# Kernel tuning notes

Measured on AMD Instinct MI355X. Metric: run time of the kernel, lower is better.

The kernel has to match this reference:

```python
import jax, jax.numpy as jnp
import numpy as np


def setup_inputs() -> dict:
    key = jax.random.key(0)
    kq, kk, kv = jax.random.split(key, 3)
    B, H, S, D = 4, 16, 2048, 64
    Q = jax.random.normal(kq, (B, H, S, D), dtype=jnp.float32)
    K = jax.random.normal(kk, (B, H, S, D), dtype=jnp.float32)
    V = jax.random.normal(kv, (B, H, S, D), dtype=jnp.float32)
    return {"Q": Q, "K": K, "V": V}


def reference(Q, K, V):
    # Faithful to the source: scale = d**(-2); scores = (Q @ K^T) / scale
    # i.e. scores are MULTIPLIED by d^2 (quirk of the original module).
    d = K.shape[-1]
    scale = jnp.asarray(d, Q.dtype) ** (-2)
    scores = jnp.einsum('bhqd,bhkd->bhqk', Q, K) / scale  # [B,H,S,S]
    attn = jax.nn.softmax(scores, axis=-1)
    out = jnp.einsum('bhqk,bhkd->bhqd', attn, V)
    return out
```

## Files before the change

### kernel.cpp

```cpp
#include <hip/hip_runtime.h>
#include <math.h>


#define S_LEN 2048
#define D_DIM 64
#define NH 64
#define BM 128
#define BN 64
#define QTILES (S_LEN / BM)
#define KTILES (S_LEN / BN)

typedef unsigned short u16;
typedef unsigned int u32;
typedef _Float16 f16;
typedef __attribute__((ext_vector_type(8))) _Float16 f16x8;
typedef __attribute__((ext_vector_type(2))) __fp16 fp16x2;
typedef __attribute__((ext_vector_type(4))) float f32x4;

#define SC_FULL (4096.0f * 1.4426950408889634f)
#define QSCALE (SC_FULL / 64.0f)
#define KSCALE 64.0f

union f16cv { f16 h; u16 u; };
union pkcv { fp16x2 h; u32 u; };

__device__ __forceinline__ void split2h(float a, u16& hi, u16& lo) {
  f16cv ch, cl;
  ch.h = (f16)a;
  float r = a - (float)ch.h;
  cl.h = (f16)r;
  hi = ch.u; lo = cl.u;
}

__device__ __forceinline__ int swz(int row, int chunk) {
  return (row << 6) + ((chunk ^ (row & 7)) << 3);
}

__global__ void prep_kernel(const float* __restrict__ K, const float* __restrict__ V,
                            u16* __restrict__ Kh, u16* __restrict__ Km,
                            u16* __restrict__ Vt) {
  if (blockIdx.x < 8192) {
    size_t i4 = ((size_t)blockIdx.x * 256 + threadIdx.x) * 4;
    float4 v = *(const float4*)(K + i4);
    u16 h0, l0, h1, l1, h2, l2, h3, l3;
    split2h(v.x * KSCALE, h0, l0);
    split2h(v.y * KSCALE, h1, l1);
    split2h(v.z * KSCALE, h2, l2);
    split2h(v.w * KSCALE, h3, l3);
    *(uint2*)(Kh + i4) = make_uint2((u32)h0 | ((u32)h1 << 16), (u32)h2 | ((u32)h3 << 16));
    *(uint2*)(Km + i4) = make_uint2((u32)l0 | ((u32)l1 << 16), (u32)l2 | ((u32)l3 << 16));
  } else {
    __shared__ float Vf[64 * 65];
    const int idx = blockIdx.x - 8192;
    const int kt = idx & 31, h = idx >> 5;
    const int tid = threadIdx.x;
    const float* V0 = V + ((size_t)h * S_LEN + kt * 64) * 64;
    const int tx = tid & 15, ty = tid >> 4;
#pragma unroll
    for (int p = 0; p < 4; ++p) {
      int r = ty + 16 * p;
      float4 v = *(const float4*)(V0 + r * 64 + tx * 4);
      Vf[r * 65 + 4 * tx + 0] = v.x;
      Vf[r * 65 + 4 * tx + 1] = v.y;
      Vf[r * 65 + 4 * tx + 2] = v.z;
      Vf[r * 65 + 4 * tx + 3] = v.w;
    }
    __syncthreads();
    const int ch = tid & 7, dr = tid >> 3;
#pragma unroll
    for (int p = 0; p < 2; ++p) {
      int d = dr + 32 * p;
      u32 w[4];
#pragma unroll
      for (int i = 0; i < 4; ++i) {
        f16cv a, b;
        a.h = (f16)Vf[(8 * ch + 2 * i) * 65 + d];
        b.h = (f16)Vf[(8 * ch + 2 * i + 1) * 65 + d];
        w[i] = (u32)a.u | ((u32)b.u << 16);
      }
      size_t o = ((size_t)h * 64 + d) * S_LEN + (size_t)kt * 64 + 8 * ch;
      *(uint4*)(Vt + o) = make_uint4(w[0], w[1], w[2], w[3]);
    }
  }
}

#define K0_B 0
#define K1_B 4096
#define VT_B 8192
#define P_B  12288
#define LDS_USH 20480

__global__ __launch_bounds__(256, 3)
void attn_mfma_f16(const float* __restrict__ Q, const u16* __restrict__ Kh,
                   const u16* __restrict__ Km, const u16* __restrict__ Vt,
                   float* __restrict__ O) {
  __shared__ __align__(16) u16 lds[LDS_USH];

  const int tid = threadIdx.x;
  const int lane = tid & 63;
  const int wv = tid >> 6;
  const int c = lane & 15;
  const int g = lane >> 4;
  const int h = blockIdx.x;
  const int qtile = blockIdx.y;

  f16x8 aqh[2][2], aqm[2][2];
#pragma unroll
  for (int m = 0; m < 2; ++m) {
    int qrow = qtile * BM + wv * 32 + m * 16 + c;
    const float* qp = Q + ((size_t)h * S_LEN + qrow) * 64 + g * 8;
#pragma unroll
    for (int ks = 0; ks < 2; ++ks) {
      float4 a = *(const float4*)(qp + ks * 32);
      float4 b = *(const float4*)(qp + ks * 32 + 4);
      float v[8] = {a.x, a.y, a.z, a.w, b.x, b.y, b.z, b.w};
      f16x8 hi, lo;
#pragma unroll
      for (int e = 0; e < 8; ++e) {
        float q = v[e] * QSCALE;
        f16 qh = (f16)q;
        hi[e] = qh;
        lo[e] = (f16)(q - (float)qh);
      }
      aqh[m][ks] = hi; aqm[m][ks] = lo;
    }
  }

  f32x4 Oacc[2][4];
  float mrow[2] = {-INFINITY, -INFINITY};
  float lrow[2] = {0.f, 0.f};
#pragma unroll
  for (int m = 0; m < 2; ++m)
#pragma unroll
    for (int t = 0; t < 4; ++t) Oacc[m][t] = (f32x4){0.f, 0.f, 0.f, 0.f};

  const int srow = tid >> 2;
  const int c0 = tid & 3;
  const int d0a = swz(srow, c0), d0b = swz(srow, c0 + 4);
  const size_t gKbase = ((size_t)h * S_LEN + srow) * 64 + c0 * 8;
  const size_t gVbase = ((size_t)h * 64 + srow) * S_LEN + c0 * 8;

  uint4 rk0a = *(const uint4*)(Kh + gKbase);
  uint4 rk0b = *(const uint4*)(Kh + gKbase + 32);
  uint4 rk1a = *(const uint4*)(Km + gKbase);
  uint4 rk1b = *(const uint4*)(Km + gKbase + 32);
  uint4 rva  = *(const uint4*)(Vt + gVbase);
  uint4 rvb  = *(const uint4*)(Vt + gVbase + 32);

  for (int kt = 0; kt < KTILES; ++kt) {
    __syncthreads();
    *(uint4*)&lds[K0_B + d0a] = rk0a;
    *(uint4*)&lds[K0_B + d0b] = rk0b;
    *(uint4*)&lds[K1_B + d0a] = rk1a;
    *(uint4*)&lds[K1_B + d0b] = rk1b;
    *(uint4*)&lds[VT_B + d0a] = rva;
    *(uint4*)&lds[VT_B + d0b] = rvb;
    __syncthreads();

    if (kt + 1 < KTILES) {
      size_t gK = gKbase + (size_t)(kt + 1) * BN * 64;
      size_t gV = gVbase + (size_t)(kt + 1) * BN;
      rk0a = *(const uint4*)(Kh + gK);
      rk0b = *(const uint4*)(Kh + gK + 32);
      rk1a = *(const uint4*)(Km + gK);
      rk1b = *(const uint4*)(Km + gK + 32);
      rva  = *(const uint4*)(Vt + gV);
      rvb  = *(const uint4*)(Vt + gV + 32);
    }

    f32x4 S[2][4];
#pragma unroll
    for (int m = 0; m < 2; ++m)
#pragma unroll
      for (int t = 0; t < 4; ++t) S[m][t] = (f32x4){0.f, 0.f, 0.f, 0.f};
#pragma unroll
    for (int ks = 0; ks < 2; ++ks) {
#pragma unroll
      for (int t = 0; t < 4; ++t) {
        int off = swz(16 * t + c, g + 4 * ks);
        f16x8 bh = *(const f16x8*)&lds[K0_B + off];
        f16x8 bm = *(const f16x8*)&lds[K1_B + off];
#pragma unroll
        for (int m = 0; m < 2; ++m) {
          S[m][t] = __builtin_amdgcn_mfma_f32_16x16x32_f16(bh, aqh[m][ks], S[m][t], 0, 0, 0);
          S[m][t] = __builtin_amdgcn_mfma_f32_16x16x32_f16(bm, aqh[m][ks], S[m][t], 0, 0, 0);
          S[m][t] = __builtin_amdgcn_mfma_f32_16x16x32_f16(bh, aqm[m][ks], S[m][t], 0, 0, 0);
        }
      }
    }

#pragma unroll
    for (int m = 0; m < 2; ++m) {
      float mx = S[m][0][0];
#pragma unroll
      for (int t = 0; t < 4; ++t)
#pragma unroll
        for (int r = 0; r < 4; ++r) mx = fmaxf(mx, S[m][t][r]);
      mx = fmaxf(mx, __shfl_xor(mx, 16));
      mx = fmaxf(mx, __shfl_xor(mx, 32));
      float mnew = fmaxf(mrow[m], mx);
      float a = exp2f(mrow[m] - mnew);
      mrow[m] = mnew;
      float ps = 0.f;
#pragma unroll
      for (int t = 0; t < 4; ++t)
#pragma unroll
        for (int r = 0; r < 4; ++r) {
          float p = exp2f(S[m][t][r] - mnew);
          S[m][t][r] = p;
          ps += p;
        }
      lrow[m] = lrow[m] * a + ps;
      float ab[4];
#pragma unroll
      for (int r = 0; r < 4; ++r) ab[r] = __shfl(a, (lane & 48) | (4 * g + r));
#pragma unroll
      for (int nt = 0; nt < 4; ++nt)
#pragma unroll
        for (int r = 0; r < 4; ++r) Oacc[m][nt][r] *= ab[r];
      int rql = wv * 32 + m * 16 + c;
      int rowbase = rql << 6;
      int rs7 = c & 7;
#pragma unroll
      for (int t = 0; t < 4; ++t) {
        pkcv p01, p23;
        p01.h = __builtin_amdgcn_cvt_pkrtz(S[m][t][0], S[m][t][1]);
        p23.h = __builtin_amdgcn_cvt_pkrtz(S[m][t][2], S[m][t][3]);
        int chunk = 2 * t + (g >> 1);
        int off = rowbase + ((chunk ^ rs7) << 3) + 4 * (g & 1);
        *(uint2*)&lds[P_B + off] = make_uint2(p01.u, p23.u);
      }
    }

    f16x8 ap[2][2];
#pragma unroll
    for (int m = 0; m < 2; ++m) {
      int rql = wv * 32 + m * 16 + c;
#pragma unroll
      for (int ks = 0; ks < 2; ++ks)
        ap[m][ks] = *(const f16x8*)&lds[P_B + swz(rql, g + 4 * ks)];
    }
#pragma unroll
    for (int ks = 0; ks < 2; ++ks) {
#pragma unroll
      for (int nt = 0; nt < 4; ++nt) {
        f16x8 bv = *(const f16x8*)&lds[VT_B + swz(16 * nt + c, g + 4 * ks)];
#pragma unroll
        for (int m = 0; m < 2; ++m)
          Oacc[m][nt] = __builtin_amdgcn_mfma_f32_16x16x32_f16(ap[m][ks], bv, Oacc[m][nt], 0, 0, 0);
      }
    }
  }

#pragma unroll
  for (int m = 0; m < 2; ++m) {
    float l = lrow[m];
    l += __shfl_xor(l, 16);
    l += __shfl_xor(l, 32);
    float linv = 1.0f / l;
    float lr[4];
#pragma unroll
    for (int r = 0; r < 4; ++r) lr[r] = __shfl(linv, (lane & 48) | (4 * g + r));
#pragma unroll
    for (int nt = 0; nt < 4; ++nt)
#pragma unroll
      for (int r = 0; r < 4; ++r) {
        int row = qtile * BM + wv * 32 + m * 16 + 4 * g + r;
        O[((size_t)h * S_LEN + row) * 64 + 16 * nt + c] = Oacc[m][nt][r] * lr[r];
      }
  }
}

#define LSTR 68
__global__ __launch_bounds__(256, 2)
void attn_fp32_kernel(const float* __restrict__ Q, const float* __restrict__ K,
                      const float* __restrict__ V, float* __restrict__ O) {
  __shared__ float Qs[64][LSTR];
  __shared__ float Ks[64][LSTR];
  __shared__ float Vs[64][LSTR];
  __shared__ float Ps[64][LSTR];
  const int tid = threadIdx.x;
  const int tx = tid & 15, ty = tid >> 4;
  const int qtile = blockIdx.x, head = blockIdx.y;
  const long hoff = (long)head * S_LEN * D_DIM;
  const float* Qp = Q + hoff + (long)qtile * 64 * D_DIM;
  const float* Kp = K + hoff;
  const float* Vp = V + hoff;
  float* Op = O + hoff + (long)qtile * 64 * D_DIM;
  {
    const int cc = tx * 4;
#pragma unroll
    for (int p = 0; p < 4; ++p) {
      const int r = ty + p * 16;
      *(float4*)(&Qs[r][cc]) = *(const float4*)(Qp + r * D_DIM + cc);
    }
  }
  float m_i[4], l_i[4];
  float4 o_acc[4];
#pragma unroll
  for (int i = 0; i < 4; ++i) {
    m_i[i] = -INFINITY; l_i[i] = 0.0f;
    o_acc[i] = make_float4(0.f, 0.f, 0.f, 0.f);
  }
  const float SCALE = 4096.0f;
  const float LOG2E = 1.4426950408889634f;
  for (int kt = 0; kt < S_LEN / 64; ++kt) {
    {
      const int cc = tx * 4;
      const float* Kt = Kp + kt * 64 * D_DIM;
      const float* Vv = Vp + kt * 64 * D_DIM;
#pragma unroll
      for (int p = 0; p < 4; ++p) {
        const int r = ty + p * 16;
        *(float4*)(&Ks[r][cc]) = *(const float4*)(Kt + r * D_DIM + cc);
        *(float4*)(&Vs[r][cc]) = *(const float4*)(Vv + r * D_DIM + cc);
      }
    }
    __syncthreads();
    float s[4][4];
#pragma unroll
    for (int i = 0; i < 4; ++i)
#pragma unroll
      for (int j = 0; j < 4; ++j) s[i][j] = 0.0f;
#pragma unroll
    for (int d = 0; d < D_DIM; d += 4) {
      float4 q4[4], k4[4];
#pragma unroll
      for (int i = 0; i < 4; ++i) q4[i] = *(const float4*)(&Qs[ty * 4 + i][d]);
#pragma unroll
      for (int j = 0; j < 4; ++j) k4[j] = *(const float4*)(&Ks[tx + 16 * j][d]);
#pragma unroll
      for (int i = 0; i < 4; ++i)
#pragma unroll
        for (int j = 0; j < 4; ++j) {
          s[i][j] += q4[i].x * k4[j].x; s[i][j] += q4[i].y * k4[j].y;
          s[i][j] += q4[i].z * k4[j].z; s[i][j] += q4[i].w * k4[j].w;
        }
    }
#pragma unroll
    for (int i = 0; i < 4; ++i) {
#pragma unroll
      for (int j = 0; j < 4; ++j) s[i][j] *= SCALE;
      float rm = fmaxf(fmaxf(s[i][0], s[i][1]), fmaxf(s[i][2], s[i][3]));
#pragma unroll
      for (int off = 8; off >= 1; off >>= 1) rm = fmaxf(rm, __shfl_xor(rm, off));
      const float mnew = fmaxf(m_i[i], rm);
      const float alpha = exp2f((m_i[i] - mnew) * LOG2E);
      float rs = 0.0f;
#pragma unroll
      for (int j = 0; j < 4; ++j) {
        const float p = exp2f((s[i][j] - mnew) * LOG2E);
        s[i][j] = p; rs += p;
      }
#pragma unroll
      for (int off = 8; off >= 1; off >>= 1) rs += __shfl_xor(rs, off);
      l_i[i] = l_i[i] * alpha + rs;
      m_i[i] = mnew;
      o_acc[i].x *= alpha; o_acc[i].y *= alpha; o_acc[i].z *= alpha; o_acc[i].w *= alpha;
      const int mm = ty * 4 + i;
      Ps[mm][tx] = s[i][0]; Ps[mm][tx + 16] = s[i][1];
      Ps[mm][tx + 32] = s[i][2]; Ps[mm][tx + 48] = s[i][3];
    }
    __syncthreads();
#pragma unroll
    for (int k = 0; k < 64; k += 4) {
      float4 p4[4], v4[4];
#pragma unroll
      for (int i = 0; i < 4; ++i) p4[i] = *(const float4*)(&Ps[ty * 4 + i][k]);
#pragma unroll
      for (int kk = 0; kk < 4; ++kk) v4[kk] = *(const float4*)(&Vs[k + kk][tx * 4]);
#pragma unroll
      for (int i = 0; i < 4; ++i) {
        o_acc[i].x += p4[i].x * v4[0].x + p4[i].y * v4[1].x + p4[i].z * v4[2].x + p4[i].w * v4[3].x;
        o_acc[i].y += p4[i].x * v4[0].y + p4[i].y * v4[1].y + p4[i].z * v4[2].y + p4[i].w * v4[3].y;
        o_acc[i].z += p4[i].x * v4[0].z + p4[i].y * v4[1].z + p4[i].z * v4[2].z + p4[i].w * v4[3].z;
        o_acc[i].w += p4[i].x * v4[0].w + p4[i].y * v4[1].w + p4[i].z * v4[2].w + p4[i].w * v4[3].w;
      }
    }
    __syncthreads();
  }
#pragma unroll
  for (int i = 0; i < 4; ++i) {
    const float inv = 1.0f / l_i[i];
    o_acc[i].x *= inv; o_acc[i].y *= inv; o_acc[i].z *= inv; o_acc[i].w *= inv;
    *(float4*)(Op + (ty * 4 + i) * D_DIM + tx * 4) = o_acc[i];
  }
}

extern "C" void kernel_launch(void* const* d_in, const int* in_sizes, int n_in,
                              void* d_out, int out_size, void* d_ws, size_t ws_size,
                              hipStream_t stream) {
  const float* Q = (const float*)d_in[0];
  const float* K = (const float*)d_in[1];
  const float* V = (const float*)d_in[2];
  float* O = (float*)d_out;

  const size_t P = (size_t)NH * S_LEN * D_DIM;
  const size_t need = 3 * P * sizeof(u16);

  if (ws_size >= need) {
    u16* w = (u16*)d_ws;
    u16 *Kh = w, *Km = w + P, *Vt = w + 2 * P;
    prep_kernel<<<8192 + 2048, 256, 0, stream>>>(K, V, Kh, Km, Vt);
    attn_mfma_f16<<<dim3(NH, QTILES), 256, 0, stream>>>(Q, Kh, Km, Vt, O);
  } else {
    attn_fp32_kernel<<<dim3(S_LEN / 64, NH), 256, 0, stream>>>(Q, K, V, O);
  }
}
```

Baseline: 298.7 us.

## Transpose PV MFMA output layout, shrink P staging LDS, raise occupancy

Swaps the MFMA operand order for the P·V product so each lane holds output values for its own query row. This removes the cross-lane shuffles for the rescale factor and the final normalisation, and allows float4 output stores. P is now staged in a smaller per-ks LDS buffer with a new swizzle, which cuts LDS from 40KB to 32KB and raises launch bounds to 4 blocks per CU. The accumulator rescale is skipped when the running max does not change. The trade-off is more interleaving of LDS writes and reads inside the ks loop, and register pressure under the higher occupancy target.

```diff
diff --git a/kernel.cpp b/kernel.cpp
--- a/kernel.cpp
+++ b/kernel.cpp
@@ -88,9 +88,9 @@
 #define K1_B 4096
 #define VT_B 8192
 #define P_B  12288
-#define LDS_USH 20480
-
-__global__ __launch_bounds__(256, 3)
+#define LDS_USH 16384
+
+__global__ __launch_bounds__(256, 4)
 void attn_mfma_f16(const float* __restrict__ Q, const u16* __restrict__ Kh,
                    const u16* __restrict__ Km, const u16* __restrict__ Vt,
                    float* __restrict__ O) {
@@ -189,6 +189,7 @@
       }
     }
 
+    u32 pkv[2][4][2];
 #pragma unroll
     for (int m = 0; m < 2; ++m) {
       float mx = S[m][0][0];
@@ -211,43 +212,47 @@
           ps += p;
         }
       lrow[m] = lrow[m] * a + ps;
-      float ab[4];
-#pragma unroll
-      for (int r = 0; r < 4; ++r) ab[r] = __shfl(a, (lane & 48) | (4 * g + r));
-#pragma unroll
-      for (int nt = 0; nt < 4; ++nt)
-#pragma unroll
-        for (int r = 0; r < 4; ++r) Oacc[m][nt][r] *= ab[r];
-      int rql = wv * 32 + m * 16 + c;
-      int rowbase = rql << 6;
-      int rs7 = c & 7;
+      if (a < 1.0f) {
+#pragma unroll
+        for (int nt = 0; nt < 4; ++nt)
+#pragma unroll
+          for (int r = 0; r < 4; ++r) Oacc[m][nt][r] *= a;
+      }
 #pragma unroll
       for (int t = 0; t < 4; ++t) {
         pkcv p01, p23;
         p01.h = __builtin_amdgcn_cvt_pkrtz(S[m][t][0], S[m][t][1]);
         p23.h = __builtin_amdgcn_cvt_pkrtz(S[m][t][2], S[m][t][3]);
-        int chunk = 2 * t + (g >> 1);
-        int off = rowbase + ((chunk ^ rs7) << 3) + 4 * (g & 1);
-        *(uint2*)&lds[P_B + off] = make_uint2(p01.u, p23.u);
-      }
-    }
-
-    f16x8 ap[2][2];
-#pragma unroll
-    for (int m = 0; m < 2; ++m) {
-      int rql = wv * 32 + m * 16 + c;
-#pragma unroll
-      for (int ks = 0; ks < 2; ++ks)
-        ap[m][ks] = *(const f16x8*)&lds[P_B + swz(rql, g + 4 * ks)];
-    }
+        pkv[m][t][0] = p01.u;
+        pkv[m][t][1] = p23.u;
+      }
+    }
+
 #pragma unroll
     for (int ks = 0; ks < 2; ++ks) {
+#pragma unroll
+      for (int m = 0; m < 2; ++m) {
+        int rql = wv * 32 + m * 16 + c;
+        int base = P_B + (rql << 5);
+#pragma unroll
+        for (int th = 0; th < 2; ++th) {
+          int t = 2 * ks + th;
+          int off = base + (((4 * th + g) ^ (c & 6)) << 2);
+          *(uint2*)&lds[off] = make_uint2(pkv[m][t][0], pkv[m][t][1]);
+        }
+      }
+      f16x8 ap[2];
+#pragma unroll
+      for (int m = 0; m < 2; ++m) {
+        int rql = wv * 32 + m * 16 + c;
+        ap[m] = *(const f16x8*)&lds[P_B + (rql << 5) + ((g ^ ((c >> 1) & 3)) << 3)];
+      }
 #pragma unroll
       for (int nt = 0; nt < 4; ++nt) {
         f16x8 bv = *(const f16x8*)&lds[VT_B + swz(16 * nt + c, g + 4 * ks)];
 #pragma unroll
         for (int m = 0; m < 2; ++m)
-          Oacc[m][nt] = __builtin_amdgcn_mfma_f32_16x16x32_f16(ap[m][ks], bv, Oacc[m][nt], 0, 0, 0);
+          Oacc[m][nt] = __builtin_amdgcn_mfma_f32_16x16x32_f16(bv, ap[m], Oacc[m][nt], 0, 0, 0);
       }
     }
   }
@@ -258,16 +263,17 @@
     l += __shfl_xor(l, 16);
     l += __shfl_xor(l, 32);
     float linv = 1.0f / l;
-    float lr[4];
-#pragma unroll
-    for (int r = 0; r < 4; ++r) lr[r] = __shfl(linv, (lane & 48) | (4 * g + r));
-#pragma unroll
-    for (int nt = 0; nt < 4; ++nt)
-#pragma unroll
-      for (int r = 0; r < 4; ++r) {
-        int row = qtile * BM + wv * 32 + m * 16 + 4 * g + r;
-        O[((size_t)h * S_LEN + row) * 64 + 16 * nt + c] = Oacc[m][nt][r] * lr[r];
-      }
+    int q = qtile * BM + wv * 32 + m * 16 + c;
+    float* op = O + ((size_t)h * S_LEN + q) * 64 + 4 * g;
+#pragma unroll
+    for (int nt = 0; nt < 4; ++nt) {
+      float4 o;
+      o.x = Oacc[m][nt][0] * linv;
+      o.y = Oacc[m][nt][1] * linv;
+      o.z = Oacc[m][nt][2] * linv;
+      o.w = Oacc[m][nt][3] * linv;
+      *(float4*)(op + 16 * nt) = o;
+    }
   }
 }
 
```

After: 479.9 us. 60.7% more time.
